# Optimization experiments

Hardware: AMD Instinct MI355X
Metric: run time of the kernel (lower is better)

The kernel has to match this reference:

```python
import jax, jax.numpy as jnp
import numpy as np

N_NODES, N_GRAPHS, PER_GRAPH, N_EDGES = 20000, 200, 100, 320000
X_DIM, E_DIM, G_DIM = 32, 16, 32
NUM_EMB, HEADS, LAYERS = 64, 2, 3
EPS_GEN, EPS_LN = 1e-7, 1e-5


def _w(k, shape, scale=0.05):
    return (jax.random.normal(k, shape) * scale).astype(jnp.float32)


def _mlp3(x, W1, b1, W2, b2, W3, b3):
    h = jax.nn.leaky_relu(x @ W1 + b1)
    h = jax.nn.leaky_relu(h @ W2 + b2)
    return h @ W3 + b3


def _seg_sum(x, idx, n):
    return jax.ops.segment_sum(x, idx, num_segments=n)


def _seg_mean(x, idx, n):
    s = _seg_sum(x, idx, n)
    cnt = _seg_sum(jnp.ones((x.shape[0],), x.dtype), idx, n)
    return s / jnp.clip(cnt, 1.0, None)[:, None]


def _seg_softmax(logits, idx, n):
    # PyG softmax: subtract per-segment max, normalize with +1e-16
    m = jax.ops.segment_max(logits, idx, num_segments=n)
    m = jnp.where(jnp.isfinite(m), m, 0.0)
    e = jnp.exp(logits - m[idx])
    s = jax.ops.segment_sum(e, idx, num_segments=n)
    return e / (s[idx] + 1e-16)


def _graph_layernorm(x, batch, n_graphs):
    # PyG LayerNorm(mode='graph', affine=False): mean/var over all node-feature
    # entries of each graph.
    f = x.shape[-1]
    cnt = _seg_sum(jnp.ones((x.shape[0],), x.dtype), batch, n_graphs)
    norm = jnp.clip(cnt, 1.0, None) * f
    mean = _seg_sum(x.sum(-1), batch, n_graphs) / norm
    xc = x - mean[batch][:, None]
    var = _seg_sum((xc * xc).sum(-1), batch, n_graphs) / norm
    return xc / jnp.sqrt(var + EPS_LN)[batch][:, None]


def _forward(x, edge_attr, cond, edge_index, batch,
             x2h_W1, x2h_b1, x2h_W2, x2h_b2, x2h_W3, x2h_b3,
             e2h_W1, e2h_b1, e2h_W2, e2h_b2, e2h_W3, e2h_b3,
             c2h_W1, c2h_b1, c2h_W2, c2h_b2, c2h_W3, c2h_b3,
             gen_W, tr_Wq, tr_bq, tr_Wk, tr_bk, tr_Wv, tr_bv, tr_We, tr_Ws, tr_bs,
             lin_W, lin_b, ff_W1, ff_b1, ff_W2, ff_b2):
    N = x.shape[0]
    G = cond.shape[0]
    Naug = N + G
    o = _mlp3(x, x2h_W1, x2h_b1, x2h_W2, x2h_b2, x2h_W3, x2h_b3)
    e = _mlp3(edge_attr, e2h_W1, e2h_b1, e2h_W2, e2h_b2, e2h_W3, e2h_b3)
    c = _mlp3(cond, c2h_W1, c2h_b1, c2h_W2, c2h_b2, c2h_W3, c2h_b3)
    # virtual-node edges: node<->virtual node of its graph (virtual ids = N..N+G-1)
    u = jnp.arange(N, dtype=edge_index.dtype)
    v = batch.astype(edge_index.dtype) + N
    aug_ei = jnp.concatenate([edge_index, jnp.stack([u, v]), jnp.stack([v, u])], axis=1)
    e_p = jnp.zeros((2 * N, NUM_EMB), o.dtype).at[:, 0].set(1.0)
    aug_e = jnp.concatenate([e, e_p], axis=0)
    # add_self_loops(fill_value='mean'): self-loop attr = mean of incoming edge attrs
    loop_attr = _seg_mean(aug_e, aug_ei[1], Naug)
    loops = jnp.arange(Naug, dtype=edge_index.dtype)
    aug_ei = jnp.concatenate([aug_ei, jnp.stack([loops, loops])], axis=1)
    aug_e = jnp.concatenate([aug_e, loop_attr], axis=0)
    aug_batch = jnp.concatenate([batch, jnp.arange(G, dtype=batch.dtype)])
    o = jnp.concatenate([o, c], axis=0)  # [Naug, emb]
    src, dst = aug_ei[0], aug_ei[1]
    scale = 1.0 / float(np.sqrt(NUM_EMB))
    for i in range(LAYERS):
        # GENConv(aggr='add', norm=None, num_layers=1): sum(relu(x_j+e)+eps) + x, then Linear
        msg = jax.nn.relu(o[src] + aug_e) + EPS_GEN
        agg = (_seg_sum(msg, dst, Naug) + o) @ gen_W[i]
        # TransformerConv(2*emb -> emb, heads, edge_dim=emb, concat=True)
        xin = jnp.concatenate([o, agg], axis=1)  # [Naug, 2*emb]
        q = (xin @ tr_Wq[i] + tr_bq[i]).reshape(Naug, HEADS, NUM_EMB)
        k = (xin @ tr_Wk[i] + tr_bk[i]).reshape(Naug, HEADS, NUM_EMB)
        vv = (xin @ tr_Wv[i] + tr_bv[i]).reshape(Naug, HEADS, NUM_EMB)
        eh = (aug_e @ tr_We[i]).reshape(-1, HEADS, NUM_EMB)  # [E, H, C]
        kj = k[src] + eh
        alpha = _seg_softmax(jnp.einsum('ehc,ehc->eh', q[dst], kj) * scale, dst, Naug)
        tout = _seg_sum((vv[src] + eh) * alpha[..., None], dst, Naug)
        tout = tout.reshape(Naug, HEADS * NUM_EMB) + xin @ tr_Ws[i] + tr_bs[i]
        # residual + graph LayerNorm, then FFN + graph LayerNorm
        o = _graph_layernorm(o + tout @ lin_W[i] + lin_b[i], aug_batch, G)
        ff = jax.nn.leaky_relu(o @ ff_W1[i] + ff_b1[i]) @ ff_W2[i] + ff_b2[i]
        o = _graph_layernorm(o + ff, aug_batch, G)
    node_o, virt = o[:N], o[N:]
    glob = jnp.concatenate([_seg_mean(node_o, batch, G), virt, c], axis=1)
    o_final = jnp.concatenate([node_o, c[batch]], axis=1)
    return (o_final, glob)


def setup_inputs() -> dict:
    key = jax.random.key(0)
    ks = iter(jax.random.split(key, 64))
    inp = {}
    inp['x'] = jax.random.normal(next(ks), (N_NODES, X_DIM), dtype=jnp.float32)
    inp['edge_attr'] = jax.random.normal(next(ks), (N_EDGES, E_DIM), dtype=jnp.float32)
    inp['cond'] = jax.random.normal(next(ks), (N_GRAPHS, G_DIM), dtype=jnp.float32)
    src = jax.random.randint(next(ks), (N_EDGES,), 0, N_NODES)
    dst = (src // PER_GRAPH) * PER_GRAPH + jax.random.randint(next(ks), (N_EDGES,), 0, PER_GRAPH)
    inp['edge_index'] = jnp.stack([src, dst]).astype(jnp.int32)
    inp['batch'] = jnp.repeat(jnp.arange(N_GRAPHS, dtype=jnp.int32), PER_GRAPH)
    for p, nin in [('x2h', X_DIM), ('e2h', E_DIM), ('c2h', G_DIM)]:
        inp[p + '_W1'] = _w(next(ks), (nin, NUM_EMB)); inp[p + '_b1'] = _w(next(ks), (NUM_EMB,))
        inp[p + '_W2'] = _w(next(ks), (NUM_EMB, NUM_EMB)); inp[p + '_b2'] = _w(next(ks), (NUM_EMB,))
        inp[p + '_W3'] = _w(next(ks), (NUM_EMB, NUM_EMB)); inp[p + '_b3'] = _w(next(ks), (NUM_EMB,))
    HC = HEADS * NUM_EMB
    inp['gen_W'] = _w(next(ks), (LAYERS, NUM_EMB, NUM_EMB))
    inp['tr_Wq'] = _w(next(ks), (LAYERS, 2 * NUM_EMB, HC)); inp['tr_bq'] = _w(next(ks), (LAYERS, HC))
    inp['tr_Wk'] = _w(next(ks), (LAYERS, 2 * NUM_EMB, HC)); inp['tr_bk'] = _w(next(ks), (LAYERS, HC))
    inp['tr_Wv'] = _w(next(ks), (LAYERS, 2 * NUM_EMB, HC)); inp['tr_bv'] = _w(next(ks), (LAYERS, HC))
    inp['tr_We'] = _w(next(ks), (LAYERS, NUM_EMB, HC))
    inp['tr_Ws'] = _w(next(ks), (LAYERS, 2 * NUM_EMB, HC)); inp['tr_bs'] = _w(next(ks), (LAYERS, HC))
    inp['lin_W'] = _w(next(ks), (LAYERS, HC, NUM_EMB)); inp['lin_b'] = _w(next(ks), (LAYERS, NUM_EMB))
    inp['ff_W1'] = _w(next(ks), (LAYERS, NUM_EMB, 4 * NUM_EMB)); inp['ff_b1'] = _w(next(ks), (LAYERS, 4 * NUM_EMB))
    inp['ff_W2'] = _w(next(ks), (LAYERS, 4 * NUM_EMB, NUM_EMB)); inp['ff_b2'] = _w(next(ks), (LAYERS, NUM_EMB))
    return inp


def reference(x, edge_attr, cond, edge_index, batch,
              x2h_W1, x2h_b1, x2h_W2, x2h_b2, x2h_W3, x2h_b3,
              e2h_W1, e2h_b1, e2h_W2, e2h_b2, e2h_W3, e2h_b3,
              c2h_W1, c2h_b1, c2h_W2, c2h_b2, c2h_W3, c2h_b3,
              gen_W, tr_Wq, tr_bq, tr_Wk, tr_bk, tr_Wv, tr_bv, tr_We, tr_Ws, tr_bs,
              lin_W, lin_b, ff_W1, ff_b1, ff_W2, ff_b2):
    return _forward(x, edge_attr, cond, edge_index, batch,
                    x2h_W1, x2h_b1, x2h_W2, x2h_b2, x2h_W3, x2h_b3,
                    e2h_W1, e2h_b1, e2h_W2, e2h_b2, e2h_W3, e2h_b3,
                    c2h_W1, c2h_b1, c2h_W2, c2h_b2, c2h_W3, c2h_b3,
                    gen_W, tr_Wq, tr_bq, tr_Wk, tr_bk, tr_Wv, tr_bv, tr_We, tr_Ws, tr_bs,
                    lin_W, lin_b, ff_W1, ff_b1, ff_W2, ff_b2)
```

## Files before the change

### kernel.cpp

```cpp
#include <hip/hip_runtime.h>
#include <cstddef>

#define NN   20000
#define NG   200
#define NE   320000
#define NAUG 20200
#define NE2  360000
#define EAUG 380200
#define DD   64
#define HC   128

typedef float  f32x4 __attribute__((ext_vector_type(4)));
typedef short  s16x8 __attribute__((ext_vector_type(8)));

static __device__ __forceinline__ unsigned short bf16r(float f){
  unsigned u = __float_as_uint(f);
  u += 0x7FFFu + ((u >> 16) & 1u);
  return (unsigned short)(u >> 16);
}
static __device__ __forceinline__ float4 b2f4(ushort4 u){
  return make_float4(__uint_as_float((unsigned)u.x << 16),
                     __uint_as_float((unsigned)u.y << 16),
                     __uint_as_float((unsigned)u.z << 16),
                     __uint_as_float((unsigned)u.w << 16));
}
static __device__ __forceinline__ ushort4 f2b4(float4 v){
  ushort4 s; s.x=bf16r(v.x); s.y=bf16r(v.y); s.z=bf16r(v.z); s.w=bf16r(v.w); return s;
}
static __device__ __forceinline__ float d4(float4 a, float4 b){
  return a.x*b.x + a.y*b.y + a.z*b.z + a.w*b.w;
}
static __device__ __forceinline__ float4 f4ab(float4 a, float s, float4 b, float t){
  return make_float4(a.x*s + b.x*t, a.y*s + b.y*t, a.z*s + b.z*t, a.w*s + b.w*t);
}
static __device__ __forceinline__ float4 f4s(float4 a, float s){
  return make_float4(a.x*s, a.y*s, a.z*s, a.w*s);
}

#define WTAB_INIT { \
  {0,0,128,128,136,128,0},{0,0,128,128,136,128,16384},{0,0,128,128,136,128,32768}, \
  {1,0,128,128,136,128,0},{1,0,128,128,136,128,16384},{1,0,128,128,136,128,32768}, \
  {2,0,128,128,136,128,0},{2,0,128,128,136,128,16384},{2,0,128,128,136,128,32768}, \
  {3,0,128,128,136,128,0},{3,0,128,128,136,128,16384},{3,0,128,128,136,128,32768}, \
  {4,0,64,64,72,64,0},{4,0,64,64,72,64,4096},{4,0,64,64,72,64,8192}, \
  {5,0,128,64,136,64,0},{5,0,128,64,136,64,8192},{5,0,128,64,136,64,16384}, \
  {6,0,64,256,72,256,0},{6,0,64,256,72,256,16384},{6,0,64,256,72,256,32768}, \
  {7,0,256,64,264,64,0},{7,0,256,64,264,64,16384},{7,0,256,64,264,64,32768}, \
  {8,1,64,64,72,128,0},{8,1,64,64,72,128,64},{8,1,64,64,72,128,8192},{8,1,64,64,72,128,8256},{8,1,64,64,72,128,16384},{8,1,64,64,72,128,16448}, \
  {8,0,64,64,72,128,0},{8,0,64,64,72,128,64},{8,0,64,64,72,128,8192},{8,0,64,64,72,128,8256},{8,0,64,64,72,128,16384},{8,0,64,64,72,128,16448}, \
  {9,0,32,64,40,64,0},{10,0,64,64,72,64,0},{11,0,64,64,72,64,0}, \
  {12,0,16,64,40,64,0},{13,0,64,64,72,64,0},{14,0,64,64,72,64,0}, \
  {15,0,32,64,40,64,0},{16,0,64,64,72,64,0},{17,0,64,64,72,64,0} }

static const int WTAB_H[45][7] = WTAB_INIT;
__device__ static const int WTAB_D[45][7] = WTAB_INIT;

struct WPtrs { const float* p[18]; };

__global__ void wconv_all_k(WPtrs wp, unsigned short* __restrict__ outbase){
  int b = blockIdx.x;
  int acc = 0; unsigned ooff = 0;
  #pragma unroll 1
  for (int j = 0; j < 45; j++){
    int e  = WTAB_D[j][3] * WTAB_D[j][4];
    int nb = (e + 255) >> 8;
    if (b < acc + nb){
      int idx = (b - acc)*256 + threadIdx.x;
      if (idx < e){
        int KP = WTAB_D[j][4];
        int n = idx / KP, k = idx % KP;
        float v = 0.f;
        if (k < WTAB_D[j][2]){
          const float* s = wp.p[WTAB_D[j][0]];
          int st = WTAB_D[j][5], so = WTAB_D[j][6];
          v = (WTAB_D[j][1] == 0) ? s[(size_t)so + (size_t)k*st + n]
                                  : s[(size_t)so + (size_t)n*st + k];
        }
        outbase[ooff + idx] = bf16r(v);
      }
      return;
    }
    acc += nb; ooff += (unsigned)e;
  }
}

template<int NT>
__launch_bounds__(256)
__global__ void gemm_mfma_k(const float* __restrict__ A, const float* __restrict__ A2,
                            int M, int K, int lda,
                            const unsigned short* __restrict__ WtG,
                            const float* __restrict__ bias, int act,
                            const float* __restrict__ res, const float* __restrict__ res2,
                            int rstride, float* __restrict__ out, int ostride){
  extern __shared__ unsigned short smem[];
  const int KC  = (K > 128) ? 128 : K;
  const int KPc = KC + 8;
  const int KP  = K + 8;
  unsigned short* Wts  = smem;
  unsigned short* Asub = smem + NT*KPc;
  const int tid = threadIdx.x;
  const int wid = tid >> 6, lane = tid & 63;
  const int lrow = lane & 15, quad = lane >> 4;
  const int m0 = blockIdx.x * 64;
  f32x4 acc[NT/16];
  #pragma unroll
// ... 29 lines not shown
    }
    __syncthreads();
  }

  const int mb = m0 + wid*16 + quad*4;
  #pragma unroll
  for (int nt = 0; nt < NT/16; nt++){
    int n = nt*16 + lrow;
    #pragma unroll
    for (int r = 0; r < 4; r++){
      int m = mb + r;
      if (m < M){
        float v = acc[nt][r];
        if (bias) v += bias[n];
        if (act)  v = v > 0.f ? v : 0.01f*v;
        if (res)  v += res [(size_t)m*rstride + n];
        if (res2) v += res2[(size_t)m*rstride + n];
        out[(size_t)m*ostride + n] = v;
      }
    }
  }
}

struct PW4 { const unsigned short* w[4]; const float* b[4]; };

__launch_bounds__(256)
__global__ void qkvs4_k(const float* __restrict__ A, int M, PW4 pw,
                        float* __restrict__ out){
  __shared__ __align__(16) unsigned short Wts[128*136];
  __shared__ __align__(16) unsigned short Asub[64*136];
  const unsigned short* WtG = pw.w[blockIdx.y];
  const float* bias = pw.b[blockIdx.y];
  const int tid = threadIdx.x;
  const int wid = tid >> 6, lane = tid & 63;
  const int lrow = lane & 15, quad = lane >> 4;
  const int m0 = blockIdx.x * 64;
  for (int i = tid; i < 128*17; i += 256){
    int n = i/17, c8 = i%17;
    *(uint4*)&Wts[n*136 + c8*8] = *(const uint4*)&WtG[(size_t)n*136 + c8*8];
  }
  for (int i = tid; i < 64*32; i += 256){
    int r = i >> 5, c4 = (i & 31)*4;
    int m = m0 + r;
    float4 v = make_float4(0.f,0.f,0.f,0.f);
    if (m < M) v = *(const float4*)(A + (size_t)m*128 + c4);
    *(ushort4*)&Asub[r*136 + c4] = f2b4(v);
  }
  __syncthreads();
  f32x4 acc[8];
  #pragma unroll
  for (int t=0;t<8;t++) acc[t] = (f32x4){0.f,0.f,0.f,0.f};
  #pragma unroll
  for (int ks = 0; ks < 4; ks++){
    s16x8 a = *(const s16x8*)&Asub[(wid*16 + lrow)*136 + ks*32 + quad*8];
    #pragma unroll
    for (int nt = 0; nt < 8; nt++){
      s16x8 b = *(const s16x8*)&Wts[(nt*16 + lrow)*136 + ks*32 + quad*8];
      acc[nt] = __builtin_amdgcn_mfma_f32_16x16x32_bf16(a, b, acc[nt], 0, 0, 0);
    }
  }
  const int mb = m0 + wid*16 + quad*4;
  const int yoff = blockIdx.y*128;
  #pragma unroll
  for (int nt = 0; nt < 8; nt++){
    int n = nt*16 + lrow;
    #pragma unroll
    for (int r = 0; r < 4; r++){
      int m = mb + r;
      if (m < M) out[(size_t)m*512 + yoff + n] = acc[nt][r] + bias[n];
    }
  }
}

struct PW2 { const unsigned short* w[2]; };

__launch_bounds__(256)
__global__ void qe2_k(const float* __restrict__ qkvs, int M, PW2 pw,
                      float* __restrict__ qe){
  __shared__ __align__(16) unsigned short Wts[64*72];
  __shared__ __align__(16) unsigned short Asub[64*72];
  const unsigned short* WtG = pw.w[blockIdx.y];
  const int tid = threadIdx.x;
  const int wid = tid >> 6, lane = tid & 63;
  const int lrow = lane & 15, quad = lane >> 4;
  const int m0 = blockIdx.x * 64;
  const int yoff = blockIdx.y * 64;
  for (int i = tid; i < 64*9; i += 256){
    int n = i/9, c8 = i%9;
    *(uint4*)&Wts[n*72 + c8*8] = *(const uint4*)&WtG[(size_t)n*72 + c8*8];
  }
  for (int i = tid; i < 64*16; i += 256){
    int r = i >> 4, c4 = (i & 15)*4;
    int m = m0 + r;
    float4 v = make_float4(0.f,0.f,0.f,0.f);
    if (m < M) v = *(const float4*)(qkvs + (size_t)m*512 + yoff + c4);
    *(ushort4*)&Asub[r*72 + c4] = f2b4(v);
  }
  __syncthreads();
  f32x4 acc[4];
  #pragma unroll
  for (int t=0;t<4;t++) acc[t] = (f32x4){0.f,0.f,0.f,0.f};
  #pragma unroll
  for (int ks = 0; ks < 2; ks++){
    s16x8 a = *(const s16x8*)&Asub[(wid*16 + lrow)*72 + ks*32 + quad*8];
    #pragma unroll
    for (int nt = 0; nt < 4; nt++){
      s16x8 b = *(const s16x8*)&Wts[(nt*16 + lrow)*72 + ks*32 + quad*8];
      acc[nt] = __builtin_amdgcn_mfma_f32_16x16x32_bf16(a, b, acc[nt], 0, 0, 0);
    }
  }
  const int mb = m0 + wid*16 + quad*4;
  #pragma unroll
  for (int nt = 0; nt < 4; nt++){
    int n = nt*16 + lrow;
    #pragma unroll
    for (int r = 0; r < 4; r++){
      int m = mb + r;
      if (m < M) qe[(size_t)m*HC + yoff + n] = acc[nt][r];
    }
  }
}

__launch_bounds__(256)
__global__ void tout2_k(const float* __restrict__ wv, int M, PW2 pw,
                        const float* __restrict__ t1, const float* __restrict__ qkvs,
                        float* __restrict__ tout){
  __shared__ __align__(16) unsigned short Wts[64*72];
  __shared__ __align__(16) unsigned short Asub[64*72];
  const unsigned short* WtG = pw.w[blockIdx.y];
  const int tid = threadIdx.x;
  const int wid = tid >> 6, lane = tid & 63;
  const int lrow = lane & 15, quad = lane >> 4;
  const int m0 = blockIdx.x * 64;
  const int yoff = blockIdx.y * 64;
  for (int i = tid; i < 64*9; i += 256){
    int n = i/9, c8 = i%9;
    *(uint4*)&Wts[n*72 + c8*8] = *(const uint4*)&WtG[(size_t)n*72 + c8*8];
  }
  for (int i = tid; i < 64*16; i += 256){
    int r = i >> 4, c4 = (i & 15)*4;
    int m = m0 + r;
    float4 v = make_float4(0.f,0.f,0.f,0.f);
    if (m < M) v = *(const float4*)(wv + (size_t)m*HC + yoff + c4);
    *(ushort4*)&Asub[r*72 + c4] = f2b4(v);
  }
  __syncthreads();
  f32x4 acc[4];
  #pragma unroll
  for (int t=0;t<4;t++) acc[t] = (f32x4){0.f,0.f,0.f,0.f};
  #pragma unroll
  for (int ks = 0; ks < 2; ks++){
    s16x8 a = *(const s16x8*)&Asub[(wid*16 + lrow)*72 + ks*32 + quad*8];
    #pragma unroll
    for (int nt = 0; nt < 4; nt++){
      s16x8 b = *(const s16x8*)&Wts[(nt*16 + lrow)*72 + ks*32 + quad*8];
      acc[nt] = __builtin_amdgcn_mfma_f32_16x16x32_bf16(a, b, acc[nt], 0, 0, 0);
    }
  }
  const int mb = m0 + wid*16 + quad*4;
  #pragma unroll
  for (int nt = 0; nt < 4; nt++){
    int n = nt*16 + lrow;
    #pragma unroll
    for (int r = 0; r < 4; r++){
      int m = mb + r;
      if (m < M)
        tout[(size_t)m*HC + yoff + n] = acc[nt][r]
          + t1[(size_t)m*HC + yoff + n] + qkvs[(size_t)m*512 + 384 + yoff + n];
    }
  }
}

__launch_bounds__(256)
__global__ void mlp3_mfma_k(const float* __restrict__ X, int M, int Din,
                            const unsigned short* __restrict__ w1t,
                            const unsigned short* __restrict__ w2t,
                            const unsigned short* __restrict__ w3t,
                            const float* __restrict__ b1, const float* __restrict__ b2,
                            const float* __restrict__ b3,
                            const int* __restrict__ perm, float* __restrict__ out,
                            unsigned short* __restrict__ outb){
  __shared__ __align__(16) unsigned short W1s[64*40], W2s[64*72], W3s[64*72];
  __shared__ __align__(16) unsigned short xs[64*40], hs[64*72];
  __shared__ float bsh[192];
  const int tid = threadIdx.x;
  for (int i = tid; i < 320; i += 256)  *(uint4*)&W1s[i*8] = *(const uint4*)&w1t[i*8];
  for (int i = tid; i < 576; i += 256){ *(uint4*)&W2s[i*8] = *(const uint4*)&w2t[i*8];
                                        *(uint4*)&W3s[i*8] = *(const uint4*)&w3t[i*8]; }
  if (tid < 64){ bsh[tid] = b1[tid]; bsh[64+tid] = b2[tid]; bsh[128+tid] = b3[tid]; }
  const int m0 = blockIdx.x * 64;
  for (int i = tid; i < 512; i += 256){
// ... 103 lines not shown
  int tid = threadIdx.x;
  const int per = (NAUG + 1023) / 1024;
  int base = tid * per;
  int s = 0;
  for (int i=0;i<per;i++){ int idx=base+i; if (idx<NAUG) s += cnt[idx]; }
  part[tid] = s;
  __syncthreads();
  for (int off=1; off<1024; off<<=1){
    int v = (tid>=off) ? part[tid-off] : 0;
    __syncthreads();
    part[tid] += v;
    __syncthreads();
  }
  int run = (tid==0) ? 0 : part[tid-1];
  for (int i=0;i<per;i++){
    int idx=base+i;
    if (idx<NAUG){ rowptr[idx]=run; run += cnt[idx]; }
  }
  if (tid==0) rowptr[NAUG] = EAUG;
}

__global__ void scatter_k(const int* __restrict__ srcA, const int* __restrict__ dstA,
                          const int* __restrict__ rowptr, int* __restrict__ cursor,
                          int* __restrict__ eid, int* __restrict__ esrc,
                          int* __restrict__ epos, int* __restrict__ pdst){
  int e = blockIdx.x*256 + threadIdx.x;
  if (e >= EAUG) return;
  int d = dstA[e];
  int pos = rowptr[d] + atomicAdd(&cursor[d], 1);
  eid[pos]  = e;
  esrc[pos] = srcA[e];
  pdst[pos] = d;
  epos[e]   = pos;
}

__global__ void set_ep_k(const int* __restrict__ epos, unsigned short* __restrict__ aug_b){
  int idx = blockIdx.x*256 + threadIdx.x;
  if (idx >= 2*NN*DD) return;
  int i = idx >> 6, c = idx & 63;
  aug_b[(size_t)epos[NE + i]*DD + c] = (c==0) ? (unsigned short)0x3F80 : (unsigned short)0;
}

__launch_bounds__(256)
__global__ void loopmean_k(const int* __restrict__ rowptr, const int* __restrict__ eid,
                           const int* __restrict__ epos, unsigned short* __restrict__ aug_b){
  int tid = threadIdx.x;
  int d = blockIdx.x*16 + (tid>>4);
  if (d >= NAUG) return;
  int t4 = (tid & 15)*4;
  int beg = rowptr[d], end = rowptr[d+1];
  float4 s = make_float4(0.f,0.f,0.f,0.f); int n = 0;
  for (int p=beg; p<end; p++){
    int e = eid[p];
    if (e < NE2){
      float4 a = b2f4(*(const ushort4*)(aug_b + (size_t)p*DD + t4));
      s.x += a.x; s.y += a.y; s.z += a.z; s.w += a.w;
      n++;
    }
  }
  float cv = (n < 1) ? 1.f : (float)n;
  *(ushort4*)(aug_b + (size_t)epos[NE2+d]*DD + t4) = f2b4(f4s(s, 1.f/cv));
}

__launch_bounds__(512)
__global__ void msg_graph_k(const float* __restrict__ o, const unsigned short* __restrict__ aug_b,
                            const int* __restrict__ rowptr,
                            const int* __restrict__ esrc, float* __restrict__ aggsum){
  __shared__ __align__(16) float OS[101*72];
  __shared__ unsigned char EL[3072];
  const int g = blockIdx.x >> 1, half = blockIdx.x & 1;
  const int tid = threadIdx.x;
  for (int i = tid; i < 101*16; i += 512){
    int ln = i >> 4, c4 = (i & 15)*4;
    int row = (ln < 100) ? g*100 + ln : NN + g;
    *(float4*)&OS[ln*72 + c4] = *(const float4*)(o + (size_t)row*DD + c4);
  }
  const int baseA = rowptr[g*100];
  const int lenA  = rowptr[g*100 + 100] - baseA;
  const int baseB = rowptr[NN + g];
  const int lenB  = rowptr[NN + g + 1] - baseB;
  const bool useL = (lenA + lenB) <= 3072;
  if (useL){
    for (int i = tid; i < lenA; i += 512){
      int s = esrc[baseA + i];
// ... 15 lines not shown
    for (int p = pbeg; p < pend; p++){
      int ls;
      if (useL) ls = EL[p + eofs];
      else { int s = esrc[p]; ls = (s >= NN) ? 100 : (s - g*100); }
      float4 ov = *(const float4*)&OS[ls*72 + t4];
      float4 ae = b2f4(*(const ushort4*)(aug_b + (size_t)p*DD + t4));
      acc.x += fmaxf(ov.x+ae.x, 0.f) + 1e-7f;
      acc.y += fmaxf(ov.y+ae.y, 0.f) + 1e-7f;
      acc.z += fmaxf(ov.z+ae.z, 0.f) + 1e-7f;
      acc.w += fmaxf(ov.w+ae.w, 0.f) + 1e-7f;
    }
    *(float4*)(aggsum + (size_t)d*DD + t4) = acc;
  }
}

__global__ void copy_o_xin_k(const float* __restrict__ o, float* __restrict__ xin){
  int idx = blockIdx.x*256 + threadIdx.x;
  if (idx >= NAUG*DD) return;
  int n = idx >> 6, c = idx & 63;
  xin[(size_t)n*HC + c] = o[idx];
}

__launch_bounds__(512)
__global__ void scoredot_k(const float* __restrict__ qkvs, const float* __restrict__ qe,
                           const unsigned short* __restrict__ aug_b,
                           const int* __restrict__ pdst, const int* __restrict__ esrc,
                           float2* __restrict__ lg){
  int p = blockIdx.x*32 + (threadIdx.x >> 4);
  if (p >= EAUG) return;
  int t4 = (threadIdx.x & 15)*4;
  int d = pdst[p], s = esrc[p];
  const float* qr = qkvs + (size_t)d*512;
  const float* kr = qkvs + (size_t)s*512 + 128;
  float4 q0  = *(const float4*)(qr + t4);
  float4 q1  = *(const float4*)(qr + 64 + t4);
  float4 qe0 = *(const float4*)(qe + (size_t)d*HC + t4);
  float4 qe1 = *(const float4*)(qe + (size_t)d*HC + 64 + t4);
  float4 k0  = *(const float4*)(kr + t4);
  float4 k1  = *(const float4*)(kr + 64 + t4);
  float4 ae  = b2f4(*(const ushort4*)(aug_b + (size_t)p*DD + t4));
  float p0 = d4(q0,k0) + d4(qe0,ae);
  float p1 = d4(q1,k1) + d4(qe1,ae);
  p0 += __shfl_xor(p0,8); p0 += __shfl_xor(p0,4); p0 += __shfl_xor(p0,2); p0 += __shfl_xor(p0,1);
  p1 += __shfl_xor(p1,8); p1 += __shfl_xor(p1,4); p1 += __shfl_xor(p1,2); p1 += __shfl_xor(p1,1);
  if ((threadIdx.x & 15) == 0) lg[p] = make_float2(p0*0.125f, p1*0.125f);
}

__launch_bounds__(512)
__global__ void attn_lite_k(const float* __restrict__ qkvs, const float2* __restrict__ lg,
                            const int* __restrict__ rowptr, const int* __restrict__ esrc,
                            float* __restrict__ t1, float2* __restrict__ m2,
                            float2* __restrict__ linv2){
  __shared__ __align__(16) unsigned short VS[101*128];
  __shared__ unsigned char EL[3072];
  const int g = blockIdx.x >> 1, half = blockIdx.x & 1;
  const int tid = threadIdx.x;
  for (int i = tid; i < 101*32; i += 512){
    int ln = i >> 5, c4 = (i & 31)*4;
    int row = (ln < 100) ? g*100 + ln : NN + g;
    float4 v = *(const float4*)(qkvs + (size_t)row*512 + 256 + c4);
    *(ushort4*)&VS[ln*128 + c4] = f2b4(v);
  }
  const int baseA = rowptr[g*100];
  const int lenA  = rowptr[g*100 + 100] - baseA;
  const int baseB = rowptr[NN + g];
  const int lenB  = rowptr[NN + g + 1] - baseB;
  const bool useL = (lenA + lenB) <= 3072;
  if (useL){
    for (int i = tid; i < lenA; i += 512){
      int s = esrc[baseA + i];
      EL[i] = (unsigned char)((s >= NN) ? 100 : (s - g*100));
    }
    for (int i = tid; i < lenB; i += 512){
      int s = esrc[baseB + i];
      EL[lenA + i] = (unsigned char)((s >= NN) ? 100 : (s - g*100));
    }
  }
  __syncthreads();
  const int gr = tid >> 4, t4 = (tid & 15)*4;
  const int ld0 = half ? 51 : 0, ld1 = half ? 101 : 51;
  for (int ld = ld0 + gr; ld < ld1; ld += 32){
    int d, pbeg, pend, eofs;
    if (ld < 100){ d = g*100 + ld; pbeg = rowptr[d]; pend = rowptr[d+1]; eofs = -baseA; }
    else         { d = NN + g;     pbeg = baseB;     pend = baseB + lenB; eofs = lenA - baseB; }
    float m0=-1e30f, m1=-1e30f, l0=0.f, l1=0.f;
    float4 a0 = make_float4(0.f,0.f,0.f,0.f), a1 = a0;
    float2 lv = lg[pbeg];
    for (int p = pbeg; p < pend; p++){
      float2 nxt = (p+1 < pend) ? lg[p+1] : make_float2(0.f,0.f);
      int ls;
      if (useL) ls = EL[p + eofs];
      else { int s = esrc[p]; ls = (s >= NN) ? 100 : (s - g*100); }
      const unsigned short* vr = &VS[ls*128];
      float4 v0 = b2f4(*(const ushort4*)(vr + t4));
      float4 v1 = b2f4(*(const ushort4*)(vr + 64 + t4));
      float nm0 = fmaxf(m0, lv.x);
      float sc0 = __expf(m0 - nm0);
      float e0  = __expf(lv.x - nm0);
      l0 = l0*sc0 + e0; a0 = f4ab(a0, sc0, v0, e0); m0 = nm0;
      float nm1 = fmaxf(m1, lv.y);
      float sc1 = __expf(m1 - nm1);
      float e1  = __expf(lv.y - nm1);
      l1 = l1*sc1 + e1; a1 = f4ab(a1, sc1, v1, e1); m1 = nm1;
      lv = nxt;
    }
    float i0 = 1.f/(l0 + 1e-16f), i1 = 1.f/(l1 + 1e-16f);
    *(float4*)(t1 + (size_t)d*HC + t4)      = f4s(a0, i0);
    *(float4*)(t1 + (size_t)d*HC + 64 + t4) = f4s(a1, i1);
    if ((tid & 15) == 0){
      m2[d]    = make_float2(m0, m1);
      linv2[d] = make_float2(i0, i1);
    }
  }
}

__launch_bounds__(256)
__global__ void wsum_k(const unsigned short* __restrict__ aug_b, const float2* __restrict__ lg,
                       const float2* __restrict__ m2, const float2* __restrict__ linv2,
                       const int* __restrict__ rowptr, float* __restrict__ wbuf){
  int tid = threadIdx.x;
  int d = blockIdx.x*16 + (tid>>4);
  if (d >= NAUG) return;
  int t4 = (tid & 15)*4;
  float2 m = m2[d], li = linv2[d];
  float4 w0 = make_float4(0.f,0.f,0.f,0.f), w1 = w0;
  int beg = rowptr[d], end = rowptr[d+1];
  for (int p = beg; p < end; p++){
    float2 lv = lg[p];
    float4 ae = b2f4(*(const ushort4*)(aug_b + (size_t)p*DD + t4));
    float a0 = __expf(lv.x - m.x) * li.x;
    float a1 = __expf(lv.y - m.y) * li.y;
    w0.x += a0*ae.x; w0.y += a0*ae.y; w0.z += a0*ae.z; w0.w += a0*ae.w;
    w1.x += a1*ae.x; w1.y += a1*ae.y; w1.z += a1*ae.z; w1.w += a1*ae.w;
  }
  *(float4*)(wbuf + (size_t)d*HC + t4)      = w0;
  *(float4*)(wbuf + (size_t)d*HC + 64 + t4) = w1;
}

__global__ void ln_k(const float* __restrict__ y, float* __restrict__ o){
  int g = blockIdx.x, tid = threadIdx.x;
  float sum=0.f, ss=0.f;
  for (int i=tid; i<101*64; i+=256){
    int nd=i>>6, c=i&63;
    int row = (nd<100) ? g*100+nd : NN+g;
    float v = y[(size_t)row*DD + c];
    sum += v; ss += v*v;
  }
  #pragma unroll
  for (int off=32; off; off>>=1){ sum += __shfl_xor(sum, off); ss += __shfl_xor(ss, off); }
  __shared__ float s1[4], s2[4];
  if ((tid&63)==0){ s1[tid>>6]=sum; s2[tid>>6]=ss; }
  __syncthreads();
  sum = s1[0]+s1[1]+s1[2]+s1[3];
  ss  = s2[0]+s2[1]+s2[2]+s2[3];
  const float inv = 1.f/6464.f;
  float mean = sum*inv;
  float var  = ss*inv - mean*mean;
  float rstd = rsqrtf(var + 1e-5f);
  for (int i=tid; i<101*64; i+=256){
    int nd=i>>6, c=i&63;
    int row = (nd<100) ? g*100+nd : NN+g;
    o[(size_t)row*DD + c] = (y[(size_t)row*DD + c] - mean)*rstd;
  }
}

__global__ void copy_c_o_k(const float* __restrict__ c_emb, float* __restrict__ o){
  int idx = blockIdx.x*256 + threadIdx.x;
  if (idx >= NG*DD) return;
  o[(size_t)NN*DD + idx] = c_emb[idx];
}

__global__ void glob_k(const float* __restrict__ o, const float* __restrict__ c_emb,
                       float* __restrict__ gout){
  int g = blockIdx.x, c = threadIdx.x;
  float acc = 0.f;
  for (int t=0;t<100;t++) acc += o[(size_t)(g*100+t)*DD + c];
  gout[(size_t)g*192 + c]       = acc / 100.f;
  gout[(size_t)g*192 + 64 + c]  = o[(size_t)(NN+g)*DD + c];
  gout[(size_t)g*192 + 128 + c] = c_emb[(size_t)g*DD + c];
}
__global__ void ofinal_k(const float* __restrict__ o, const float* __restrict__ c_emb,
                         const int* __restrict__ batch, float* __restrict__ out){
  int idx = blockIdx.x*256 + threadIdx.x;
  if (idx >= NN*HC) return;
  int n = idx>>7, j = idx&127;
// ... 35 lines not shown
             * eW3=(const float*)d_in[15], *eb3=(const float*)d_in[16];
  const float* cW1=(const float*)d_in[17], *cb1=(const float*)d_in[18],
             * cW2=(const float*)d_in[19], *cb2=(const float*)d_in[20],
             * cW3=(const float*)d_in[21], *cb3=(const float*)d_in[22];
  const float* gen_W=(const float*)d_in[23];
  const float* trWq=(const float*)d_in[24], *trbq=(const float*)d_in[25];
  const float* trWk=(const float*)d_in[26], *trbk=(const float*)d_in[27];
  const float* trWv=(const float*)d_in[28], *trbv=(const float*)d_in[29];
  const float* trWe=(const float*)d_in[30];
  const float* trWs=(const float*)d_in[31], *trbs=(const float*)d_in[32];
  const float* linW=(const float*)d_in[33], *linb=(const float*)d_in[34];
  const float* ffW1=(const float*)d_in[35], *ffb1=(const float*)d_in[36];
  const float* ffW2=(const float*)d_in[37], *ffb2=(const float*)d_in[38];
  float* out = (float*)d_out;

  float* ws = (float*)d_ws;
  size_t off = 0;
  auto alloc = [&](size_t n)->float*{ float* p = ws + off; off += (n + 63) & ~(size_t)63; return p; };
  int*      srcA  = (int*)alloc(EAUG);
  int*      dstA  = (int*)alloc(EAUG);
  int*      cnt   = (int*)alloc(NAUG);
  int*      rowptr= (int*)alloc(NAUG+1);
  int*      cursor= (int*)alloc(NAUG);
  int*      eid   = (int*)alloc(EAUG);
  int*      esrc  = (int*)alloc(EAUG);
  int*      epos  = (int*)alloc(EAUG);
  int*      pdst  = (int*)alloc(EAUG);
  unsigned short* aug_b = (unsigned short*)alloc((size_t)EAUG*DD/2);
  float*    o     = alloc((size_t)NAUG*DD);
  float*    c_emb = alloc((size_t)NG*DD);
  float*    ybuf  = alloc((size_t)NAUG*DD);
  float*    aggsum= alloc((size_t)NAUG*DD);
  float*    xin   = alloc((size_t)NAUG*HC);
  float*    xqkvs = alloc((size_t)NAUG*512);
  float*    qeb   = alloc((size_t)NAUG*HC);
  float*    toutb = alloc((size_t)NAUG*HC);
  float*    t1    = alloc((size_t)NAUG*HC);
  float*    wbuf  = alloc((size_t)NAUG*HC);
  float*    ffh   = alloc((size_t)NAUG*256);
  float2*   lgb   = (float2*)alloc((size_t)EAUG*2);
  float2*   m2v   = (float2*)alloc((size_t)NAUG*2);
  float2*   li2v  = (float2*)alloc((size_t)NAUG*2);
  unsigned short* warena = (unsigned short*)alloc(222720);
  if (off*sizeof(float) > ws_size) return;

  const unsigned short* wptr[45];
  int wblk = 0;
  { size_t woff = 0;
    for (int j = 0; j < 45; j++){
      wptr[j] = warena + woff;
      int e = WTAB_H[j][3]*WTAB_H[j][4];
      woff += (size_t)e;
      wblk += cdiv(e, 256);
    } }

  WPtrs wp;
  wp.p[0]=trWq; wp.p[1]=trWk; wp.p[2]=trWv; wp.p[3]=trWs; wp.p[4]=gen_W;
  wp.p[5]=linW; wp.p[6]=ffW1; wp.p[7]=ffW2; wp.p[8]=trWe;
  wp.p[9]=xW1; wp.p[10]=xW2; wp.p[11]=xW3;
  wp.p[12]=eW1; wp.p[13]=eW2; wp.p[14]=eW3;
  wp.p[15]=cW1; wp.p[16]=cW2; wp.p[17]=cW3;
  wconv_all_k<<<wblk,256,0,stream>>>(wp, warena);

  build_edges_k<<<cdiv(EAUG,256),256,0,stream>>>(edge_index, batch, srcA, dstA);
  hipMemsetAsync(cnt, 0, sizeof(int)*NAUG, stream);
  hipMemsetAsync(cursor, 0, sizeof(int)*NAUG, stream);
  count_k<<<cdiv(EAUG,256),256,0,stream>>>(dstA, cnt);
  scan_k<<<1,1024,0,stream>>>(cnt, rowptr);
  scatter_k<<<cdiv(EAUG,256),256,0,stream>>>(srcA, dstA, rowptr, cursor, eid, esrc, epos, pdst);

  mlp3_mfma_k<<<cdiv(NN,64),256,0,stream>>>(x,        NN, 32, wptr[36],wptr[37],wptr[38], xb1,xb2,xb3, nullptr, o,     nullptr);
  mlp3_mfma_k<<<cdiv(NG,64),256,0,stream>>>(cond,     NG, 32, wptr[42],wptr[43],wptr[44], cb1,cb2,cb3, nullptr, c_emb, nullptr);
  mlp3_mfma_k<<<cdiv(NE,64),256,0,stream>>>(edge_attr,NE, 16, wptr[39],wptr[40],wptr[41], eb1,eb2,eb3, epos,    nullptr, aug_b);
  set_ep_k<<<cdiv(2*NN*DD,256),256,0,stream>>>(epos, aug_b);
  loopmean_k<<<cdiv(NAUG,16),256,0,stream>>>(rowptr, eid, epos, aug_b);
  copy_c_o_k<<<cdiv(NG*DD,256),256,0,stream>>>(c_emb, o);

  for (int L=0; L<3; L++){
    const float* lb_i = linb + (size_t)L*DD;
    const float* f1b  = ffb1 + (size_t)L*256;
    const float* f2b  = ffb2 + (size_t)L*DD;
    const unsigned short* genT = wptr[12+L], *linT = wptr[15+L], *ff1T = wptr[18+L], *ff2T = wptr[21+L];
    PW4 pw4; pw4.w[0]=wptr[0+L]; pw4.w[1]=wptr[3+L]; pw4.w[2]=wptr[6+L]; pw4.w[3]=wptr[9+L];
    pw4.b[0]=trbq+(size_t)L*HC; pw4.b[1]=trbk+(size_t)L*HC;
    pw4.b[2]=trbv+(size_t)L*HC; pw4.b[3]=trbs+(size_t)L*HC;
    PW2 pwE; pwE.w[0]=wptr[24+2*L]; pwE.w[1]=wptr[25+2*L];
    PW2 pwT; pwT.w[0]=wptr[30+2*L]; pwT.w[1]=wptr[31+2*L];

    msg_graph_k<<<2*NG,512,0,stream>>>(o, aug_b, rowptr, esrc, aggsum);
    copy_o_xin_k<<<cdiv(NAUG*DD,256),256,0,stream>>>(o, xin);
    gemm_mfma( 64, aggsum, o, NAUG, 64, 64, genT, nullptr, 0, nullptr, nullptr, 0, xin+64, HC, stream);
    qkvs4_k<<<dim3(cdiv(NAUG,64),4),256,0,stream>>>(xin, NAUG, pw4, xqkvs);
    qe2_k<<<dim3(cdiv(NAUG,64),2),256,0,stream>>>(xqkvs, NAUG, pwE, qeb);
    scoredot_k<<<cdiv(EAUG,32),512,0,stream>>>(xqkvs, qeb, aug_b, pdst, esrc, lgb);
    attn_lite_k<<<2*NG,512,0,stream>>>(xqkvs, lgb, rowptr, esrc, t1, m2v, li2v);
    wsum_k<<<cdiv(NAUG,16),256,0,stream>>>(aug_b, lgb, m2v, li2v, rowptr, wbuf);
    tout2_k<<<dim3(cdiv(NAUG,64),2),256,0,stream>>>(wbuf, NAUG, pwT, t1, xqkvs, toutb);
    gemm_mfma( 64, toutb, nullptr, NAUG, 128, 128, linT, lb_i, 0, o, nullptr, DD, ybuf, DD, stream);
    ln_k<<<NG,256,0,stream>>>(ybuf, o);
    gemm_mfma(256, o,   nullptr, NAUG,  64,  64, ff1T, f1b, 1, nullptr, nullptr, 0, ffh, 256, stream);
    gemm_mfma( 64, ffh, nullptr, NAUG, 256, 256, ff2T, f2b, 0, o, nullptr, DD, ybuf, DD, stream);
    ln_k<<<NG,256,0,stream>>>(ybuf, o);
  }

  glob_k<<<NG,64,0,stream>>>(o, c_emb, out + (size_t)NN*HC);
  ofinal_k<<<cdiv(NN*HC,256),256,0,stream>>>(o, c_emb, batch, out);
}
```

Measured before the change: 1.338 ms.

## Fold edge projection into Q weights, fuse qe into QKVS GEMM, simplify softmax

Precomputes Wq·We and bq·We per layer so the query-edge projection becomes a fifth output block of the QKVS GEMM, removing the separate qe2 kernel and its buffer. The attention kernel switches from an online softmax to a two-pass max-then-sum, which rereads the logits but drops the per-edge rescaling exps. The loop-mean kernel drops the eid indirection by using the known self-loop position, and the copy of o into xin is folded into the final layernorm write of each layer. The weight fold changes rounding because the combined product is cast to bf16 once.

Result: no change. 1.316 ms (-1.6%).

```diff
diff --git a/kernel.cpp b/kernel.cpp
--- a/kernel.cpp
+++ b/kernel.cpp
@@ -9,6 +9,7 @@
 #define EAUG 380200
 #define DD   64
 #define HC   128
+#define QS   640
 
 typedef float  f32x4 __attribute__((ext_vector_type(4)));
 typedef short  s16x8 __attribute__((ext_vector_type(8)));
@@ -30,8 +31,8 @@
 static __device__ __forceinline__ float d4(float4 a, float4 b){
   return a.x*b.x + a.y*b.y + a.z*b.z + a.w*b.w;
 }
-static __device__ __forceinline__ float4 f4ab(float4 a, float s, float4 b, float t){
-  return make_float4(a.x*s + b.x*t, a.y*s + b.y*t, a.z*s + b.z*t, a.w*s + b.w*t);
+static __device__ __forceinline__ float4 f4a(float4 a, float4 b, float t){
+  return make_float4(a.x + b.x*t, a.y + b.y*t, a.z + b.z*t, a.w + b.w*t);
 }
 static __device__ __forceinline__ float4 f4s(float4 a, float s){
   return make_float4(a.x*s, a.y*s, a.z*s, a.w*s);
@@ -46,14 +47,13 @@
   {5,0,128,64,136,64,0},{5,0,128,64,136,64,8192},{5,0,128,64,136,64,16384}, \
   {6,0,64,256,72,256,0},{6,0,64,256,72,256,16384},{6,0,64,256,72,256,32768}, \
   {7,0,256,64,264,64,0},{7,0,256,64,264,64,16384},{7,0,256,64,264,64,32768}, \
-  {8,1,64,64,72,128,0},{8,1,64,64,72,128,64},{8,1,64,64,72,128,8192},{8,1,64,64,72,128,8256},{8,1,64,64,72,128,16384},{8,1,64,64,72,128,16448}, \
   {8,0,64,64,72,128,0},{8,0,64,64,72,128,64},{8,0,64,64,72,128,8192},{8,0,64,64,72,128,8256},{8,0,64,64,72,128,16384},{8,0,64,64,72,128,16448}, \
   {9,0,32,64,40,64,0},{10,0,64,64,72,64,0},{11,0,64,64,72,64,0}, \
   {12,0,16,64,40,64,0},{13,0,64,64,72,64,0},{14,0,64,64,72,64,0}, \
   {15,0,32,64,40,64,0},{16,0,64,64,72,64,0},{17,0,64,64,72,64,0} }
 
-static const int WTAB_H[45][7] = WTAB_INIT;
-__device__ static const int WTAB_D[45][7] = WTAB_INIT;
+static const int WTAB_H[39][7] = WTAB_INIT;
+__device__ static const int WTAB_D[39][7] = WTAB_INIT;
 
 struct WPtrs { const float* p[18]; };
 
@@ -61,7 +61,7 @@
   int b = blockIdx.x;
   int acc = 0; unsigned ooff = 0;
   #pragma unroll 1
-  for (int j = 0; j < 45; j++){
+  for (int j = 0; j < 39; j++){
     int e  = WTAB_D[j][3] * WTAB_D[j][4];
     int nb = (e + 255) >> 8;
     if (b < acc + nb){
@@ -81,6 +81,28 @@
       return;
     }
     acc += nb; ooff += (unsigned)e;
+  }
+}
+
+__global__ void qecomb_k(const float* __restrict__ trWq, const float* __restrict__ trbq,
+                         const float* __restrict__ trWe,
+                         unsigned short* __restrict__ qweb, float* __restrict__ bqeb){
+  int L = blockIdx.y;
+  int n = blockIdx.x;
+  int i = threadIdx.x;
+  int h = n >> 6, d = n & 63;
+  const float* Wq = trWq + (size_t)L*128*128;
+  const float* We = trWe + (size_t)L*64*128;
+  float acc = 0.f;
+  for (int c = 0; c < 64; c++)
+    acc += Wq[(size_t)i*128 + h*64 + c] * We[(size_t)d*128 + h*64 + c];
+  qweb[(size_t)L*128*136 + n*136 + i] = bf16r(acc);
+  if (i < 8) qweb[(size_t)L*128*136 + n*136 + 128 + i] = 0;
+  if (i == 0){
+    const float* bq = trbq + (size_t)L*128;
+    float b = 0.f;
+    for (int c = 0; c < 64; c++) b += bq[h*64 + c] * We[(size_t)d*128 + h*64 + c];
+    bqeb[L*128 + n] = b;
   }
 }
 
@@ -156,10 +178,10 @@
   }
 }
 
-struct PW4 { const unsigned short* w[4]; const float* b[4]; };
+struct PW5 { const unsigned short* w[5]; const float* b[5]; };
 
 __launch_bounds__(256)
-__global__ void qkvs4_k(const float* __restrict__ A, int M, PW4 pw,
+__global__ void qkvs5_k(const float* __restrict__ A, int M, PW5 pw,
                         float* __restrict__ out){
   __shared__ __align__(16) unsigned short Wts[128*136];
   __shared__ __align__(16) unsigned short Asub[64*136];
@@ -201,59 +223,12 @@
     #pragma unroll
     for (int r = 0; r < 4; r++){
       int m = mb + r;
-      if (m < M) out[(size_t)m*512 + yoff + n] = acc[nt][r] + bias[n];
+      if (m < M) out[(size_t)m*QS + yoff + n] = acc[nt][r] + bias[n];
     }
   }
 }
 
 struct PW2 { const unsigned short* w[2]; };
-
-__launch_bounds__(256)
-__global__ void qe2_k(const float* __restrict__ qkvs, int M, PW2 pw,
-                      float* __restrict__ qe){
-  __shared__ __align__(16) unsigned short Wts[64*72];
-  __shared__ __align__(16) unsigned short Asub[64*72];
-  const unsigned short* WtG = pw.w[blockIdx.y];
-  const int tid = threadIdx.x;
-  const int wid = tid >> 6, lane = tid & 63;
-  const int lrow = lane & 15, quad = lane >> 4;
-  const int m0 = blockIdx.x * 64;
-  const int yoff = blockIdx.y * 64;
-  for (int i = tid; i < 64*9; i += 256){
-    int n = i/9, c8 = i%9;
-    *(uint4*)&Wts[n*72 + c8*8] = *(const uint4*)&WtG[(size_t)n*72 + c8*8];
-  }
-  for (int i = tid; i < 64*16; i += 256){
-    int r = i >> 4, c4 = (i & 15)*4;
-    int m = m0 + r;
-    float4 v = make_float4(0.f,0.f,0.f,0.f);
-    if (m < M) v = *(const float4*)(qkvs + (size_t)m*512 + yoff + c4);
-    *(ushort4*)&Asub[r*72 + c4] = f2b4(v);
-  }
-  __syncthreads();
-  f32x4 acc[4];
-  #pragma unroll
-  for (int t=0;t<4;t++) acc[t] = (f32x4){0.f,0.f,0.f,0.f};
-  #pragma unroll
-  for (int ks = 0; ks < 2; ks++){
-    s16x8 a = *(const s16x8*)&Asub[(wid*16 + lrow)*72 + ks*32 + quad*8];
-    #pragma unroll
-    for (int nt = 0; nt < 4; nt++){
-      s16x8 b = *(const s16x8*)&Wts[(nt*16 + lrow)*72 + ks*32 + quad*8];
-      acc[nt] = __builtin_amdgcn_mfma_f32_16x16x32_bf16(a, b, acc[nt], 0, 0, 0);
-    }
-  }
-  const int mb = m0 + wid*16 + quad*4;
-  #pragma unroll
-  for (int nt = 0; nt < 4; nt++){
-    int n = nt*16 + lrow;
-    #pragma unroll
-    for (int r = 0; r < 4; r++){
-      int m = mb + r;
-      if (m < M) qe[(size_t)m*HC + yoff + n] = acc[nt][r];
-    }
-  }
-}
 
 __launch_bounds__(256)
 __global__ void tout2_k(const float* __restrict__ wv, int M, PW2 pw,
@@ -300,7 +275,7 @@
       int m = mb + r;
       if (m < M)
         tout[(size_t)m*HC + yoff + n] = acc[nt][r]
-          + t1[(size_t)m*HC + yoff + n] + qkvs[(size_t)m*512 + 384 + yoff + n];
+          + t1[(size_t)m*HC + yoff + n] + qkvs[(size_t)m*QS + 384 + yoff + n];
     }
   }
 }
@@ -450,13 +425,12 @@
 
 __global__ void scatter_k(const int* __restrict__ srcA, const int* __restrict__ dstA,
                           const int* __restrict__ rowptr, int* __restrict__ cursor,
-                          int* __restrict__ eid, int* __restrict__ esrc,
-                          int* __restrict__ epos, int* __restrict__ pdst){
+                          int* __restrict__ esrc, int* __restrict__ epos,
+                          int* __restrict__ pdst){
   int e = blockIdx.x*256 + threadIdx.x;
   if (e >= EAUG) return;
   int d = dstA[e];
   int pos = rowptr[d] + atomicAdd(&cursor[d], 1);
-  eid[pos]  = e;
   esrc[pos] = srcA[e];
   pdst[pos] = d;
   epos[e]   = pos;
@@ -470,24 +444,23 @@
 }
 
 __launch_bounds__(256)
-__global__ void loopmean_k(const int* __restrict__ rowptr, const int* __restrict__ eid,
-                           const int* __restrict__ epos, unsigned short* __restrict__ aug_b){
+__global__ void loopmean_k(const int* __restrict__ rowptr, const int* __restrict__ epos,
+                           unsigned short* __restrict__ aug_b){
   int tid = threadIdx.x;
   int d = blockIdx.x*16 + (tid>>4);
   if (d >= NAUG) return;
   int t4 = (tid & 15)*4;
   int beg = rowptr[d], end = rowptr[d+1];
-  float4 s = make_float4(0.f,0.f,0.f,0.f); int n = 0;
+  int sp = epos[NE2 + d];
+  float4 s = make_float4(0.f,0.f,0.f,0.f);
   for (int p=beg; p<end; p++){
-    int e = eid[p];
-    if (e < NE2){
-      float4 a = b2f4(*(const ushort4*)(aug_b + (size_t)p*DD + t4));
-      s.x += a.x; s.y += a.y; s.z += a.z; s.w += a.w;
-      n++;
-    }
-  }
+    float4 a = b2f4(*(const ushort4*)(aug_b + (size_t)p*DD + t4));
+    float w = (p == sp) ? 0.f : 1.f;
+    s.x += w*a.x; s.y += w*a.y; s.z += w*a.z; s.w += w*a.w;
+  }
+  int n = end - beg - 1;
   float cv = (n < 1) ? 1.f : (float)n;
-  *(ushort4*)(aug_b + (size_t)epos[NE2+d]*DD + t4) = f2b4(f4s(s, 1.f/cv));
+  *(ushort4*)(aug_b + (size_t)sp*DD + t4) = f2b4(f4s(s, 1.f/cv));
 }
 
 __launch_bounds__(512)
@@ -549,7 +522,7 @@
 }
 
 __launch_bounds__(512)
-__global__ void scoredot_k(const float* __restrict__ qkvs, const float* __restrict__ qe,
+__global__ void scoredot_k(const float* __restrict__ qkvs,
                            const unsigned short* __restrict__ aug_b,
                            const int* __restrict__ pdst, const int* __restrict__ esrc,
                            float2* __restrict__ lg){
@@ -557,12 +530,12 @@
   if (p >= EAUG) return;
   int t4 = (threadIdx.x & 15)*4;
   int d = pdst[p], s = esrc[p];
-  const float* qr = qkvs + (size_t)d*512;
-  const float* kr = qkvs + (size_t)s*512 + 128;
+  const float* qr = qkvs + (size_t)d*QS;
+  const float* kr = qkvs + (size_t)s*QS + 128;
   float4 q0  = *(const float4*)(qr + t4);
   float4 q1  = *(const float4*)(qr + 64 + t4);
-  float4 qe0 = *(const float4*)(qe + (size_t)d*HC + t4);
-  float4 qe1 = *(const float4*)(qe + (size_t)d*HC + 64 + t4);
+  float4 qe0 = *(const float4*)(qr + 512 + t4);
+  float4 qe1 = *(const float4*)(qr + 576 + t4);
   float4 k0  = *(const float4*)(kr + t4);
   float4 k1  = *(const float4*)(kr + 64 + t4);
   float4 ae  = b2f4(*(const ushort4*)(aug_b + (size_t)p*DD + t4));
@@ -585,7 +558,7 @@
   for (int i = tid; i < 101*32; i += 512){
     int ln = i >> 5, c4 = (i & 31)*4;
     int row = (ln < 100) ? g*100 + ln : NN + g;
-    float4 v = *(const float4*)(qkvs + (size_t)row*512 + 256 + c4);
+    float4 v = *(const float4*)(qkvs + (size_t)row*QS + 256 + c4);
     *(ushort4*)&VS[ln*128 + c4] = f2b4(v);
   }
   const int baseA = rowptr[g*100];
@@ -610,26 +583,25 @@
     int d, pbeg, pend, eofs;
     if (ld < 100){ d = g*100 + ld; pbeg = rowptr[d]; pend = rowptr[d+1]; eofs = -baseA; }
     else         { d = NN + g;     pbeg = baseB;     pend = baseB + lenB; eofs = lenA - baseB; }
-    float m0=-1e30f, m1=-1e30f, l0=0.f, l1=0.f;
+    float m0 = -1e30f, m1 = -1e30f;
+    for (int p = pbeg; p < pend; p++){
+      float2 lv = lg[p];
+      m0 = fmaxf(m0, lv.x); m1 = fmaxf(m1, lv.y);
+    }
+    float l0 = 0.f, l1 = 0.f;
     float4 a0 = make_float4(0.f,0.f,0.f,0.f), a1 = a0;
-    float2 lv = lg[pbeg];
     for (int p = pbeg; p < pend; p++){
-      float2 nxt = (p+1 < pend) ? lg[p+1] : make_float2(0.f,0.f);
+      float2 lv = lg[p];
       int ls;
       if (useL) ls = EL[p + eofs];
       else { int s = esrc[p]; ls = (s >= NN) ? 100 : (s - g*100); }
       const unsigned short* vr = &VS[ls*128];
       float4 v0 = b2f4(*(const ushort4*)(vr + t4));
       float4 v1 = b2f4(*(const ushort4*)(vr + 64 + t4));
-      float nm0 = fmaxf(m0, lv.x);
-      float sc0 = __expf(m0 - nm0);
-      float e0  = __expf(lv.x - nm0);
-      l0 = l0*sc0 + e0; a0 = f4ab(a0, sc0, v0, e0); m0 = nm0;
-      float nm1 = fmaxf(m1, lv.y);
-      float sc1 = __expf(m1 - nm1);
-      float e1  = __expf(lv.y - nm1);
-      l1 = l1*sc1 + e1; a1 = f4ab(a1, sc1, v1, e1); m1 = nm1;
-      lv = nxt;
+      float e0 = __expf(lv.x - m0);
+      float e1 = __expf(lv.y - m1);
+      l0 += e0; a0 = f4a(a0, v0, e0);
+      l1 += e1; a1 = f4a(a1, v1, e1);
     }
     float i0 = 1.f/(l0 + 1e-16f), i1 = 1.f/(l1 + 1e-16f);
     *(float4*)(t1 + (size_t)d*HC + t4)      = f4s(a0, i0);
@@ -649,7 +621,8 @@
   int d = blockIdx.x*16 + (tid>>4);
   if (d >= NAUG) return;
   int t4 = (tid & 15)*4;
-  float2 m = m2[d], li = linv2[d];
+  float2 m = m2[d];
+  float2 li = linv2[d];
   float4 w0 = make_float4(0.f,0.f,0.f,0.f), w1 = w0;
   int beg = rowptr[d], end = rowptr[d+1];
   for (int p = beg; p < end; p++){
@@ -657,14 +630,15 @@
     float4 ae = b2f4(*(const ushort4*)(aug_b + (size_t)p*DD + t4));
     float a0 = __expf(lv.x - m.x) * li.x;
     float a1 = __expf(lv.y - m.y) * li.y;
-    w0.x += a0*ae.x; w0.y += a0*ae.y; w0.z += a0*ae.z; w0.w += a0*ae.w;
-    w1.x += a1*ae.x; w1.y += a1*ae.y; w1.z += a1*ae.z; w1.w += a1*ae.w;
+    w0 = f4a(w0, ae, a0);
+    w1 = f4a(w1, ae, a1);
   }
   *(float4*)(wbuf + (size_t)d*HC + t4)      = w0;
   *(float4*)(wbuf + (size_t)d*HC + 64 + t4) = w1;
 }
 
-__global__ void ln_k(const float* __restrict__ y, float* __restrict__ o){
+__global__ void ln_k(const float* __restrict__ y, float* __restrict__ o,
+                     float* __restrict__ xin){
   int g = blockIdx.x, tid = threadIdx.x;
   float sum=0.f, ss=0.f;
   for (int i=tid; i<101*64; i+=256){
@@ -687,7 +661,9 @@
   for (int i=tid; i<101*64; i+=256){
     int nd=i>>6, c=i&63;
     int row = (nd<100) ? g*100+nd : NN+g;
-    o[(size_t)row*DD + c] = (y[(size_t)row*DD + c] - mean)*rstd;
+    float v = (y[(size_t)row*DD + c] - mean)*rstd;
+    o[(size_t)row*DD + c] = v;
+    if (xin) xin[(size_t)row*HC + c] = v;
   }
 }
 
@@ -769,7 +745,6 @@
   int*      cnt   = (int*)alloc(NAUG);
   int*      rowptr= (int*)alloc(NAUG+1);
   int*      cursor= (int*)alloc(NAUG);
-  int*      eid   = (int*)alloc(EAUG);
   int*      esrc  = (int*)alloc(EAUG);
   int*      epos  = (int*)alloc(EAUG);
   int*      pdst  = (int*)alloc(EAUG);
@@ -779,8 +754,7 @@
   float*    ybuf  = alloc((size_t)NAUG*DD);
   float*    aggsum= alloc((size_t)NAUG*DD);
   float*    xin   = alloc((size_t)NAUG*HC);
-  float*    xqkvs = alloc((size_t)NAUG*512);
-  float*    qeb   = alloc((size_t)NAUG*HC);
+  float*    xqkvs = alloc((size_t)NAUG*QS);
   float*    toutb = alloc((size_t)NAUG*HC);
   float*    t1    = alloc((size_t)NAUG*HC);
   float*    wbuf  = alloc((size_t)NAUG*HC);
@@ -788,13 +762,15 @@
   float2*   lgb   = (float2*)alloc((size_t)EAUG*2);
   float2*   m2v   = (float2*)alloc((size_t)NAUG*2);
   float2*   li2v  = (float2*)alloc((size_t)NAUG*2);
-  unsigned short* warena = (unsigned short*)alloc(222720);
+  unsigned short* warena = (unsigned short*)alloc(210432);
+  unsigned short* qweb   = (unsigned short*)alloc(3*128*136/2 + 64);
+  float*    bqeb  = alloc(3*128);
   if (off*sizeof(float) > ws_size) return;
 
-  const unsigned short* wptr[45];
+  const unsigned short* wptr[39];
   int wblk = 0;
   { size_t woff = 0;
-    for (int j = 0; j < 45; j++){
+    for (int j = 0; j < 39; j++){
       wptr[j] = warena + woff;
       int e = WTAB_H[j][3]*WTAB_H[j][4];
       woff += (size_t)e;
@@ -808,46 +784,48 @@
   wp.p[12]=eW1; wp.p[13]=eW2; wp.p[14]=eW3;
   wp.p[15]=cW1; wp.p[16]=cW2; wp.p[17]=cW3;
   wconv_all_k<<<wblk,256,0,stream>>>(wp, warena);
+  qecomb_k<<<dim3(128,3),128,0,stream>>>(trWq, trbq, trWe, qweb, bqeb);
 
   build_edges_k<<<cdiv(EAUG,256),256,0,stream>>>(edge_index, batch, srcA, dstA);
   hipMemsetAsync(cnt, 0, sizeof(int)*NAUG, stream);
   hipMemsetAsync(cursor, 0, sizeof(int)*NAUG, stream);
   count_k<<<cdiv(EAUG,256),256,0,stream>>>(dstA, cnt);
   scan_k<<<1,1024,0,stream>>>(cnt, rowptr);
-  scatter_k<<<cdiv(EAUG,256),256,0,stream>>>(srcA, dstA, rowptr, cursor, eid, esrc, epos, pdst);
-
-  mlp3_mfma_k<<<cdiv(NN,64),256,0,stream>>>(x,        NN, 32, wptr[36],wptr[37],wptr[38], xb1,xb2,xb3, nullptr, o,     nullptr);
-  mlp3_mfma_k<<<cdiv(NG,64),256,0,stream>>>(cond,     NG, 32, wptr[42],wptr[43],wptr[44], cb1,cb2,cb3, nullptr, c_emb, nullptr);
-  mlp3_mfma_k<<<cdiv(NE,64),256,0,stream>>>(edge_attr,NE, 16, wptr[39],wptr[40],wptr[41], eb1,eb2,eb3, epos,    nullptr, aug_b);
+  scatter_k<<<cdiv(EAUG,256),256,0,stream>>>(srcA, dstA, rowptr, cursor, esrc, epos, pdst);
+
+  mlp3_mfma_k<<<cdiv(NN,64),256,0,stream>>>(x,        NN, 32, wptr[30],wptr[31],wptr[32], xb1,xb2,xb3, nullptr, o,     nullptr);
+  mlp3_mfma_k<<<cdiv(NG,64),256,0,stream>>>(cond,     NG, 32, wptr[36],wptr[37],wptr[38], cb1,cb2,cb3, nullptr, c_emb, nullptr);
+  mlp3_mfma_k<<<cdiv(NE,64),256,0,stream>>>(edge_attr,NE, 16, wptr[33],wptr[34],wptr[35], eb1,eb2,eb3, epos,    nullptr, aug_b);
   set_ep_k<<<cdiv(2*NN*DD,256),256,0,stream>>>(epos, aug_b);
-  loopmean_k<<<cdiv(NAUG,16),256,0,stream>>>(rowptr, eid, epos, aug_b);
+  loopmean_k<<<cdiv(NAUG,16),256,0,stream>>>(rowptr, epos, aug_b);
   copy_c_o_k<<<cdiv(NG*DD,256),256,0,stream>>>(c_emb, o);
+  copy_o_xin_k<<<cdiv(NAUG*DD,256),256,0,stream>>>(o, xin);
 
   for (int L=0; L<3; L++){
     const float* lb_i = linb + (size_t)L*DD;
     const float* f1b  = ffb1 + (size_t)L*256;
     const float* f2b  = ffb2 + (size_t)L*DD;
     const unsigned short* genT = wptr[12+L], *linT = wptr[15+L], *ff1T = wptr[18+L], *ff2T = wptr[21+L];
-    PW4 pw4; pw4.w[0]=wptr[0+L]; pw4.w[1]=wptr[3+L]; pw4.w[2]=wptr[6+L]; pw4.w[3]=wptr[9+L];
-    pw4.b[0]=trbq+(size_t)L*HC; pw4.b[1]=trbk+(size_t)L*HC;
-    pw4.b[2]=trbv+(size_t)L*HC; pw4.b[3]=trbs+(size_t)L*HC;
-    PW2 pwE; pwE.w[0]=wptr[24+2*L]; pwE.w[1]=wptr[25+2*L];
-    PW2 pwT; pwT.w[0]=wptr[30+2*L]; pwT.w[1]=wptr[31+2*L];
+    PW5 pw5;
+    pw5.w[0]=wptr[0+L]; pw5.w[1]=wptr[3+L]; pw5.w[2]=wptr[6+L]; pw5.w[3]=wptr[9+L];
+    pw5.w[4]=qweb + (size_t)L*128*136;
+    pw5.b[0]=trbq+(size_t)L*HC; pw5.b[1]=trbk+(size_t)L*HC;
+    pw5.b[2]=trbv+(size_t)L*HC; pw5.b[3]=trbs+(size_t)L*HC;
+    pw5.b[4]=bqeb + (size_t)L*128;
+    PW2 pwT; pwT.w[0]=wptr[24+2*L]; pwT.w[1]=wptr[25+2*L];
 
     msg_graph_k<<<2*NG,512,0,stream>>>(o, aug_b, rowptr, esrc, aggsum);
-    copy_o_xin_k<<<cdiv(NAUG*DD,256),256,0,stream>>>(o, xin);
     gemm_mfma( 64, aggsum, o, NAUG, 64, 64, genT, nullptr, 0, nullptr, nullptr, 0, xin+64, HC, stream);
-    qkvs4_k<<<dim3(cdiv(NAUG,64),4),256,0,stream>>>(xin, NAUG, pw4, xqkvs);
-    qe2_k<<<dim3(cdiv(NAUG,64),2),256,0,stream>>>(xqkvs, NAUG, pwE, qeb);
-    scoredot_k<<<cdiv(EAUG,32),512,0,stream>>>(xqkvs, qeb, aug_b, pdst, esrc, lgb);
+    qkvs5_k<<<dim3(cdiv(NAUG,64),5),256,0,stream>>>(xin, NAUG, pw5, xqkvs);
+    scoredot_k<<<cdiv(EAUG,32),512,0,stream>>>(xqkvs, aug_b, pdst, esrc, lgb);
     attn_lite_k<<<2*NG,512,0,stream>>>(xqkvs, lgb, rowptr, esrc, t1, m2v, li2v);
     wsum_k<<<cdiv(NAUG,16),256,0,stream>>>(aug_b, lgb, m2v, li2v, rowptr, wbuf);
     tout2_k<<<dim3(cdiv(NAUG,64),2),256,0,stream>>>(wbuf, NAUG, pwT, t1, xqkvs, toutb);
     gemm_mfma( 64, toutb, nullptr, NAUG, 128, 128, linT, lb_i, 0, o, nullptr, DD, ybuf, DD, stream);
-    ln_k<<<NG,256,0,stream>>>(ybuf, o);
+    ln_k<<<NG,256,0,stream>>>(ybuf, o, nullptr);
     gemm_mfma(256, o,   nullptr, NAUG,  64,  64, ff1T, f1b, 1, nullptr, nullptr, 0, ffh, 256, stream);
     gemm_mfma( 64, ffh, nullptr, NAUG, 256, 256, ff2T, f2b, 0, o, nullptr, DD, ybuf, DD, stream);
-    ln_k<<<NG,256,0,stream>>>(ybuf, o);
+    ln_k<<<NG,256,0,stream>>>(ybuf, o, xin);
   }
 
   glob_k<<<NG,64,0,stream>>>(o, c_emb, out + (size_t)NN*HC);
```
